# Kernel optimization log

Measured on AMD Instinct MI355X. Metric: run time of the kernel, lower is better.

Reference implementation:

```python
import jax, jax.numpy as jnp
import numpy as np

N = 50000      # nodes
E = 800000     # edges (self-loop-free; reference appends self loops like PyG GATv2Conv)
IN = 128; H = 4; C = 64; HC = H * C; HID = 64; OUT = 2


def _gat_conv(x, wl, bl, wr, br, att, bias, src, dst, n):
    # PyG GATv2Conv: e_ij = att . leaky_relu(W_l x_j + W_r x_i); segment softmax over dst;
    # out_i = sum_j alpha_ij * (W_l x_j), heads concatenated, plus bias.
    xl = (x @ wl + bl).reshape(n, H, C)
    xr = (x @ wr + br).reshape(n, H, C)
    e = jnp.sum(att * jax.nn.leaky_relu(xl[src] + xr[dst], 0.2), axis=-1)  # [E+n, H]
    m = jax.ops.segment_max(e, dst, num_segments=n)                         # [n, H]
    ex = jnp.exp(e - m[dst])
    s = jax.ops.segment_sum(ex, dst, num_segments=n)
    alpha = ex / (s[dst] + 1e-16)
    out = jax.ops.segment_sum(xl[src] * alpha[..., None], dst, num_segments=n)
    return out.reshape(n, HC) + bias


def _graph_norm(x, w, b, ms, eps=1e-5):
    # PyG GraphNorm, single graph: normalize over all nodes
    mean = jnp.mean(x, axis=0)
    xc = x - ms * mean
    var = jnp.mean(xc * xc, axis=0)
    return w * xc / jnp.sqrt(var + eps) + b


def setup_inputs() -> dict:
    key = jax.random.key(0)
    k = jax.random.split(key, 16)
    x = jax.random.normal(k[0], (N, IN), dtype=jnp.float32)
    src = jax.random.randint(k[1], (E,), 0, N, dtype=jnp.int32)
    dst = jax.random.randint(k[2], (E,), 0, N, dtype=jnp.int32)
    dst = jnp.where(dst == src, (dst + 1) % N, dst)  # no self loops in raw edges
    edge_index = jnp.stack([src, dst])

    def lin(kk, fi, fo):
        return (jax.random.normal(kk, (fi, fo), jnp.float32) / np.float32(np.sqrt(fi)))

    zeros = lambda d: jnp.zeros((d,), jnp.float32)
    ones = lambda d: jnp.ones((d,), jnp.float32)
    return dict(
        x=x, edge_index=edge_index,
        conv0_wl=lin(k[3], IN, HC), conv0_bl=zeros(HC),
        conv0_wr=lin(k[4], IN, HC), conv0_br=zeros(HC),
        conv0_att=jax.random.normal(k[5], (H, C), jnp.float32) / np.float32(np.sqrt(C)),
        conv0_bias=zeros(HC),
        conv1_wl=lin(k[6], HC, HC), conv1_bl=zeros(HC),
        conv1_wr=lin(k[7], HC, HC), conv1_br=zeros(HC),
        conv1_att=jax.random.normal(k[8], (H, C), jnp.float32) / np.float32(np.sqrt(C)),
        conv1_bias=zeros(HC),
        gn0_w=ones(HC), gn0_b=zeros(HC), gn0_ms=ones(HC),
        gn1_w=ones(HC), gn1_b=zeros(HC), gn1_ms=ones(HC),
        lin0_w=lin(k[9], HC, HID), lin0_b=zeros(HID),
        lin1_w=lin(k[10], HID, HID), lin1_b=zeros(HID),
        lin2_w=lin(k[11], HID, OUT), lin2_b=zeros(OUT),
    )


def reference(x, edge_index, conv0_wl, conv0_bl, conv0_wr, conv0_br, conv0_att, conv0_bias,
              conv1_wl, conv1_bl, conv1_wr, conv1_br, conv1_att, conv1_bias,
              gn0_w, gn0_b, gn0_ms, gn1_w, gn1_b, gn1_ms,
              lin0_w, lin0_b, lin1_w, lin1_b, lin2_w, lin2_b):
    n = x.shape[0]
    loop = jnp.arange(n, dtype=edge_index.dtype)
    src = jnp.concatenate([edge_index[0], loop])  # add self loops (PyG default)
    dst = jnp.concatenate([edge_index[1], loop])
    # NOTE: original forward zips convs (3) with norms (2) -> only 2 convs execute.
    h = _gat_conv(x, conv0_wl, conv0_bl, conv0_wr, conv0_br, conv0_att, conv0_bias, src, dst, n)
    h = jax.nn.relu(_graph_norm(h, gn0_w, gn0_b, gn0_ms))
    h = _gat_conv(h, conv1_wl, conv1_bl, conv1_wr, conv1_br, conv1_att, conv1_bias, src, dst, n)
    h = jax.nn.relu(_graph_norm(h, gn1_w, gn1_b, gn1_ms))
    h = jax.nn.relu(h @ lin0_w + lin0_b)  # dropout_rate=None -> no dropout
    h = jax.nn.relu(h @ lin1_w + lin1_b)
    return h @ lin2_w + lin2_b
```

## Files before the change

### kernel.cpp

```cpp
#include <hip/hip_runtime.h>
#include <hip/hip_bf16.h>


typedef __bf16 bf16x8 __attribute__((ext_vector_type(8)));
typedef float  f32x4  __attribute__((ext_vector_type(4)));

__device__ __forceinline__ unsigned short f2b(float f) {
    unsigned u = __float_as_uint(f);
    return (unsigned short)((u + 0x7fffu + ((u >> 16) & 1u)) >> 16);
}

__device__ __forceinline__ unsigned pk_norm(unsigned u, float a0, float a1,
                                            float c0, float c1) {
    float lo = __uint_as_float(u << 16);
    float hi = __uint_as_float(u & 0xffff0000u);
    lo = fmaxf(fmaf(a0, lo, c0), 0.f);
    hi = fmaxf(fmaf(a1, hi, c1), 0.f);
    unsigned r;
    asm volatile("v_cvt_pk_bf16_f32 %0, %1, %2" : "=v"(r) : "v"(lo), "v"(hi));
    return r;
}

__global__ __launch_bounds__(256) void prep_all(
    const float* __restrict__ x, unsigned short* __restrict__ xbf, int nx4,
    const float* __restrict__ w0l, const float* __restrict__ w0r, unsigned short* __restrict__ Wt0,
    const float* __restrict__ w1l, const float* __restrict__ w1r, unsigned short* __restrict__ Wt1,
    const float* __restrict__ l0, unsigned short* __restrict__ Lt0,
    const float* __restrict__ l1, unsigned short* __restrict__ Lt1,
    float* __restrict__ zf, int* __restrict__ hist, int nh)
{
    int t = blockIdx.x * 256 + threadIdx.x;
    if (t < 512) { zf[t] = 0.f; }
    int i = t - 512;
    if (i >= 0 && i < nh) hist[i] = 0;
    i -= nh;
    if (i >= 0 && i < nx4) {
        float4 v = ((const float4*)x)[i];
        ushort4 o = { f2b(v.x), f2b(v.y), f2b(v.z), f2b(v.w) };
        ((ushort4*)xbf)[i] = o;
    }
    i -= nx4;
    if (i >= 0 && i < 32768) { int nn = i >> 7, kk = i & 127; Wt0[i] = f2b(w0l[kk * 256 + nn]); }
    i -= 32768;
    if (i >= 0 && i < 32768) { int nn = i >> 7, kk = i & 127; Wt0[32768 + i] = f2b(w0r[kk * 256 + nn]); }
    i -= 32768;
    if (i >= 0 && i < 65536) { int nn = i >> 8, kk = i & 255; Wt1[i] = f2b(w1l[kk * 256 + nn]); }
    i -= 65536;
    if (i >= 0 && i < 65536) { int nn = i >> 8, kk = i & 255; Wt1[65536 + i] = f2b(w1r[kk * 256 + nn]); }
    i -= 65536;
    if (i >= 0 && i < 16384) { int nn = i >> 8, kk = i & 255; Lt0[i] = f2b(l0[kk * 64 + nn]); }
    i -= 16384;
    if (i >= 0 && i < 4096)  { int nn = i >> 6, kk = i & 63;  Lt1[i] = f2b(l1[kk * 64 + nn]); }
}

template<int K, bool RELU, bool NORM>
__global__ __launch_bounds__(256) void mfma_gemm(
    const unsigned short* __restrict__ A, const unsigned short* __restrict__ Bt,
    const float* __restrict__ bias0, const float* __restrict__ bias1, int split,
    const float* __restrict__ na, const float* __restrict__ nc,
    unsigned short* __restrict__ C, int M, int N, int nt)
{
    __shared__ unsigned short cs[256][72];

    const int nwg = gridDim.x;
    const int bid = blockIdx.x;
    const int q = nwg >> 3, r = nwg & 7;
    const int xcd = bid & 7, pos = bid >> 3;
    const int wgid = (xcd < r ? xcd * (q + 1) : r * (q + 1) + (xcd - r) * q) + pos;
    const int tm = wgid / nt;
    const int tn = wgid - tm * nt;

    const int lane = threadIdx.x & 63;
    const int w = threadIdx.x >> 6;
    const int bm = tm * 256 + w * 64;
    const int bn = tn * 64;
    const int lr = lane & 15;
    const int g  = lane >> 4;
    const int lk = g * 8;

    f32x4 acc[4][4] = {};
    const unsigned short* pa[4];
    #pragma unroll
    for (int mi = 0; mi < 4; ++mi) {
        int rr = bm + mi * 16 + lr;
        if (rr >= M) rr = M - 1;
        pa[mi] = A + (size_t)rr * K + lk;
    }
    const unsigned short* pb = Bt + (size_t)(bn + lr) * K + lk;

    #pragma unroll
    for (int k0 = 0; k0 < K; k0 += 32) {
        bf16x8 bfr[4], afr[4];
        #pragma unroll
        for (int ni = 0; ni < 4; ++ni)
            bfr[ni] = *(const bf16x8*)(pb + (size_t)ni * 16 * K + k0);
        if constexpr (NORM) {
            const float4 av0 = *(const float4*)(na + k0 + lk);
            const float4 av1 = *(const float4*)(na + k0 + lk + 4);
            const float4 cv0 = *(const float4*)(nc + k0 + lk);
            const float4 cv1 = *(const float4*)(nc + k0 + lk + 4);
            #pragma unroll
            for (int mi = 0; mi < 4; ++mi) {
                uint4 u = *(const uint4*)(pa[mi] + k0);
                uint4 rr;
                rr.x = pk_norm(u.x, av0.x, av0.y, cv0.x, cv0.y);
                rr.y = pk_norm(u.y, av0.z, av0.w, cv0.z, cv0.w);
                rr.z = pk_norm(u.z, av1.x, av1.y, cv1.x, cv1.y);
                rr.w = pk_norm(u.w, av1.z, av1.w, cv1.z, cv1.w);
                afr[mi] = __builtin_bit_cast(bf16x8, rr);
            }
        } else {
            #pragma unroll
            for (int mi = 0; mi < 4; ++mi)
                afr[mi] = *(const bf16x8*)(pa[mi] + k0);
        }
        #pragma unroll
        for (int mi = 0; mi < 4; ++mi)
            #pragma unroll
            for (int ni = 0; ni < 4; ++ni)
                acc[mi][ni] = __builtin_amdgcn_mfma_f32_16x16x32_bf16(
                    bfr[ni], afr[mi], acc[mi][ni], 0, 0, 0);
    }

    #pragma unroll
    for (int ni = 0; ni < 4; ++ni) {
        const int colbase = bn + ni * 16 + g * 4;
        const float4 bv = (colbase < split)
            ? *(const float4*)(bias0 + colbase)
            : *(const float4*)(bias1 + (colbase - split));
        #pragma unroll
        for (int mi = 0; mi < 4; ++mi) {
            float v0 = acc[mi][ni][0] + bv.x;
            float v1 = acc[mi][ni][1] + bv.y;
            float v2 = acc[mi][ni][2] + bv.z;
            float v3 = acc[mi][ni][3] + bv.w;
            if (RELU) {
                v0 = fmaxf(v0, 0.f); v1 = fmaxf(v1, 0.f);
                v2 = fmaxf(v2, 0.f); v3 = fmaxf(v3, 0.f);
            }
            ushort4 o = { f2b(v0), f2b(v1), f2b(v2), f2b(v3) };
            *(ushort4*)&cs[w * 64 + mi * 16 + lr][ni * 16 + g * 4] = o;
        }
    }
    __syncthreads();

    const int row32 = threadIdx.x >> 3;
    const int seg = threadIdx.x & 7;
    #pragma unroll
    for (int p = 0; p < 8; ++p) {
        const int lrow = p * 32 + row32;
        const int grow = tm * 256 + lrow;
        if (grow < M)
            *(uint4*)(C + (size_t)grow * N + bn + seg * 8) =
                *(const uint4*)&cs[lrow][seg * 8];
    }
}

__global__ void hist_kernel(const int* __restrict__ dst, int E, int* __restrict__ hist) {
    int e = blockIdx.x * 256 + threadIdx.x;
    if (e < E) atomicAdd(&hist[dst[e]], 1);
}

__global__ void blk_sum_kernel(const int* __restrict__ hist, int n, int* __restrict__ bsum) {
    __shared__ int lds[256];
    int t = threadIdx.x;
    int i = blockIdx.x * 256 + t;
    lds[t] = (i < n) ? hist[i] : 0;
    __syncthreads();
    for (int off = 128; off > 0; off >>= 1) {
        if (t < off) lds[t] += lds[t + off];
        __syncthreads();
    }
    if (t == 0) bsum[blockIdx.x] = lds[0];
}
__global__ void bsum_scan_kernel(int* __restrict__ bsum, int nblk,
                                 int* __restrict__ row_ptr, int n) {
    __shared__ int lds[256];
    int t = threadIdx.x;
    int v = (t < nblk) ? bsum[t] : 0;
    lds[t] = v;
    __syncthreads();
    for (int off = 1; off < 256; off <<= 1) {
        int u = (t >= off) ? lds[t - off] : 0;
        __syncthreads();
        lds[t] += u;
        __syncthreads();
    }
    if (t < nblk) bsum[t] = lds[t] - v;
    if (t == 255) row_ptr[n] = lds[255];
}
__global__ void final_scan_kernel(const int* __restrict__ hist, const int* __restrict__ bsum,
                                  int n, int* __restrict__ row_ptr, int* __restrict__ cursor) {
    __shared__ int lds[256];
    int t = threadIdx.x;
    int i = blockIdx.x * 256 + t;
    int v = (i < n) ? hist[i] : 0;
    lds[t] = v;
    __syncthreads();
    for (int off = 1; off < 256; off <<= 1) {
        int u = (t >= off) ? lds[t - off] : 0;
        __syncthreads();
        lds[t] += u;
        __syncthreads();
    }
    if (i < n) {
        int ex = bsum[blockIdx.x] + lds[t] - v;
        row_ptr[i] = ex;
        cursor[i] = ex;
    }
}

__global__ void scatter_kernel(const int* __restrict__ src, const int* __restrict__ dst,
                               int E, int* cursor, int* __restrict__ esrc)
{
    int e = blockIdx.x * 256 + threadIdx.x;
    if (e < E) {
        int pos = atomicAdd(&cursor[dst[e]], 1);
        esrc[pos] = src[e];
    }
}

template<int CTRL>
__device__ __forceinline__ float dppadd(float v) {
    return v + __int_as_float(__builtin_amdgcn_update_dpp(
        0, __float_as_int(v), CTRL, 0xf, 0xf, true));
}
__device__ __forceinline__ float red8(float v) {
    v = dppadd<0xB1>(v);
    v = dppadd<0x4E>(v);
    v = dppadd<0x141>(v);
    return v;
}
__device__ __forceinline__ f32x4 unpA(uint4 u) {
    f32x4 r;
    r.x = __uint_as_float(u.x << 16); r.y = __uint_as_float(u.y << 16);
    r.z = __uint_as_float(u.z << 16); r.w = __uint_as_float(u.w << 16);
    return r;
}
__device__ __forceinline__ f32x4 unpB(uint4 u) {
    f32x4 r;
    r.x = __uint_as_float(u.x & 0xffff0000u); r.y = __uint_as_float(u.y & 0xffff0000u);
    r.z = __uint_as_float(u.z & 0xffff0000u); r.w = __uint_as_float(u.w & 0xffff0000u);
    return r;
}

__global__ __launch_bounds__(256) void gat_aggregate(
    const unsigned short* __restrict__ xlr, const float* __restrict__ att,
    const int* __restrict__ row_ptr, const int* __restrict__ esrc,
    const float* __restrict__ bias, unsigned short* __restrict__ out, int n)
{
    const int lane = threadIdx.x & 63;
    const int node = __builtin_amdgcn_readfirstlane(blockIdx.x * 4 + (threadIdx.x >> 6));
    if (node >= n) return;
    const int sub = lane & 31;
    const int half = lane >> 5;
    const int c8 = sub * 8;

    const float LOG2E = 1.4426950408889634f;
    const float4 a0 = *(const float4*)(att + c8);
    const float4 a1 = *(const float4*)(att + c8 + 4);
    f32x4 attA = { a0.x, a0.z, a1.x, a1.z };
    f32x4 attB = { a0.y, a0.w, a1.y, a1.w };
    attA *= LOG2E; attB *= LOG2E;

    const uint4 xru = *(const uint4*)(xlr + (size_t)node * 512 + 256 + c8);
    const f32x4 xrA = unpA(xru), xrB = unpB(xru);

    float m = -1e30f, s = 0.f;
    f32x4 accA = {}, accB = {};

    const int start = row_ptr[node];
    const int cnt = row_ptr[node + 1] - start + 1;
    const int kmax = (cnt + 1) >> 1;

    int idx = half;
    int srcv = (idx == 0) ? node : ((idx < cnt) ? esrc[start + idx - 1] : node);
    uint4 nu = *(const uint4*)(xlr + (size_t)srcv * 512 + c8);

    for (int k = 0; k < kmax; ++k) {
        const f32x4 vA = unpA(nu), vB = unpB(nu);
        const float mask = (idx < cnt) ? 1.f : 0.f;
        const int idxn = idx + 2;
        const int srcn = (idxn < cnt) ? esrc[start + idxn - 1] : node;
        nu = *(const uint4*)(xlr + (size_t)srcn * 512 + c8);

        const f32x4 zA = vA + xrA, zB = vB + xrB;
        const f32x4 tA = __builtin_elementwise_max(zA, zA * 0.2f);
        const f32x4 tB = __builtin_elementwise_max(zB, zB * 0.2f);
        f32x4 p = attA * tA;
        p = __builtin_elementwise_fma(attB, tB, p);
        const float e = red8((p.x + p.z) + (p.y + p.w));

        const float d = e - m;
        if (__builtin_expect(__any(d > 8.f), 0)) {
            const float mn = fmaxf(m, e);
            const float cs = __builtin_amdgcn_exp2f(m - mn);
            const float w  = __builtin_amdgcn_exp2f(e - mn) * mask;
            s = fmaf(s, cs, w);
            const f32x4 w4 = { w, w, w, w }, cv = { cs, cs, cs, cs };
            accA = __builtin_elementwise_fma(accA, cv, w4 * vA);
            accB = __builtin_elementwise_fma(accB, cv, w4 * vB);
            m = mn;
        } else {
            const float w = __builtin_amdgcn_exp2f(d) * mask;
            s += w;
            const f32x4 w4 = { w, w, w, w };
            accA = __builtin_elementwise_fma(w4, vA, accA);
            accB = __builtin_elementwise_fma(w4, vB, accB);
        }
        idx = idxn;
    }

    const float m_o = __shfl_xor(m, 32);
    const float s_o = __shfl_xor(s, 32);
    f32x4 accAo, accBo;
    accAo.x = __shfl_xor(accA.x, 32); accAo.y = __shfl_xor(accA.y, 32);
    accAo.z = __shfl_xor(accA.z, 32); accAo.w = __shfl_xor(accA.w, 32);
    accBo.x = __shfl_xor(accB.x, 32); accBo.y = __shfl_xor(accB.y, 32);
    accBo.z = __shfl_xor(accB.z, 32); accBo.w = __shfl_xor(accB.w, 32);
    const float mn = fmaxf(m, m_o);
    const float c0 = __builtin_amdgcn_exp2f(m - mn);
    const float c1 = __builtin_amdgcn_exp2f(m_o - mn);
    const float st = s * c0 + s_o * c1;
    const float inv = 1.f / (st + 1e-16f);

    if (half == 0) {
        const f32x4 oA = (accA * c0 + accAo * c1) * inv;
        const f32x4 oB = (accB * c0 + accBo * c1) * inv;
        const float4 b0 = *(const float4*)(bias + c8);
        const float4 b1 = *(const float4*)(bias + c8 + 4);
        uint4 o;
        o.x = (unsigned)f2b(oA.x + b0.x) | ((unsigned)f2b(oB.x + b0.y) << 16);
        o.y = (unsigned)f2b(oA.y + b0.z) | ((unsigned)f2b(oB.y + b0.w) << 16);
        o.z = (unsigned)f2b(oA.z + b1.x) | ((unsigned)f2b(oB.z + b1.y) << 16);
        o.w = (unsigned)f2b(oA.w + b1.z) | ((unsigned)f2b(oB.w + b1.w) << 16);
        *(uint4*)(out + (size_t)node * 256 + c8) = o;
    }
}

__global__ __launch_bounds__(256) void colstats_bf16(
    const unsigned short* __restrict__ x, int n,
    float* __restrict__ sum, float* __restrict__ sumsq)
{
    const int c = threadIdx.x;
    float s = 0.f, q = 0.f;
    for (int r = blockIdx.x; r < n; r += gridDim.x) {
        float v = __uint_as_float(((unsigned)x[(size_t)r * 256 + c]) << 16);
        s += v;
        q = fmaf(v, v, q);
    }
    atomicAdd(&sum[c], s);
    atomicAdd(&sumsq[c], q);
}
__global__ void norm_finalize(float* __restrict__ sum, float* __restrict__ sumsq,
                              const float* __restrict__ w, const float* __restrict__ b,
                              const float* __restrict__ ms,
                              float* __restrict__ a, float* __restrict__ c2, float invn)
{
    int i = threadIdx.x;
    float mean = sum[i] * invn;
    float ex2 = sumsq[i] * invn;
    float m = ms[i];
    float var = ex2 - 2.f * m * mean * mean + m * m * mean * mean;
    float av = w[i] * rsqrtf(var + 1e-5f);
    a[i] = av;
    c2[i] = b[i] - av * m * mean;
    sum[i] = 0.f;
    sumsq[i] = 0.f;
}

__global__ void lin2_kernel(const unsigned short* __restrict__ h, const float* __restrict__ w,
                            const float* __restrict__ b, float* __restrict__ out, int n)
{
    int i = blockIdx.x * 256 + threadIdx.x;
    if (i >= n) return;
    float a0 = b[0], a1 = b[1];
    const unsigned short* hr = h + (size_t)i * 64;
    #pragma unroll
    for (int k = 0; k < 64; ++k) {
        float v = __uint_as_float(((unsigned)hr[k]) << 16);
        a0 = fmaf(v, w[k * 2 + 0], a0);
        a1 = fmaf(v, w[k * 2 + 1], a1);
    }
    out[i * 2 + 0] = a0;
    out[i * 2 + 1] = a1;
}

extern "C" void kernel_launch(void* const* d_in, const int* in_sizes, int n_in,
                              void* d_out, int out_size, void* d_ws, size_t ws_size,
                              hipStream_t stream)
{
    const float* x      = (const float*)d_in[0];
    const int*   eidx   = (const int*)d_in[1];
    const float* c0_wl  = (const float*)d_in[2];
    const float* c0_bl  = (const float*)d_in[3];
    const float* c0_wr  = (const float*)d_in[4];
    const float* c0_br  = (const float*)d_in[5];
    const float* c0_att = (const float*)d_in[6];
    const float* c0_bias= (const float*)d_in[7];
    const float* c1_wl  = (const float*)d_in[8];
    const float* c1_bl  = (const float*)d_in[9];
    const float* c1_wr  = (const float*)d_in[10];
    const float* c1_br  = (const float*)d_in[11];
    const float* c1_att = (const float*)d_in[12];
    const float* c1_bias= (const float*)d_in[13];
    const float* gn0_w  = (const float*)d_in[14];
    const float* gn0_b  = (const float*)d_in[15];
    const float* gn0_ms = (const float*)d_in[16];
    const float* gn1_w  = (const float*)d_in[17];
    const float* gn1_b  = (const float*)d_in[18];
    const float* gn1_ms = (const float*)d_in[19];
    const float* lin0_w = (const float*)d_in[20];
    const float* lin0_b = (const float*)d_in[21];
    const float* lin1_w = (const float*)d_in[22];
    const float* lin1_b = (const float*)d_in[23];
    const float* lin2_w = (const float*)d_in[24];
    const float* lin2_b = (const float*)d_in[25];

    const int n = in_sizes[0] / 128;
    const int E = in_sizes[1] / 2;
    const int* src = eidx;
    const int* dst = eidx + E;

    char* wsp = (char*)d_ws;
    size_t off = 0;
    auto alloc = [&](size_t bytes) -> void* {
        void* p = wsp + off;
        off = (off + bytes + 255) & ~(size_t)255;
        return p;
    };
    unsigned short* xbf  = (unsigned short*)alloc((size_t)n * 128 * 2);
    unsigned short* xlr  = (unsigned short*)alloc((size_t)n * 512 * 2);
    unsigned short* hbB  = (unsigned short*)alloc((size_t)n * 256 * 2);
    unsigned short* mbuf = (unsigned short*)alloc((size_t)n * 64 * 2);
    unsigned short* mbuf2= (unsigned short*)alloc((size_t)n * 64 * 2);
    unsigned short* Wt0  = (unsigned short*)alloc((size_t)512 * 128 * 2);
    unsigned short* Wt1  = (unsigned short*)alloc((size_t)512 * 256 * 2);
    unsigned short* Lt0  = (unsigned short*)alloc((size_t)64 * 256 * 2);
    unsigned short* Lt1  = (unsigned short*)alloc((size_t)64 * 64 * 2);
    int*   esrc    = (int*)alloc((size_t)E * 4);
    int*   row_ptr = (int*)alloc((size_t)(n + 1) * 4);
    int*   cursor  = (int*)alloc((size_t)n * 4);
    int*   hist    = (int*)alloc((size_t)n * 4);
    int*   bsum    = (int*)alloc((size_t)256 * 4);
    float* s_sum   = (float*)alloc(256 * 4);
    float* s_sq    = (float*)alloc(256 * 4);
    float* s_a     = (float*)alloc(256 * 4);
    float* s_c     = (float*)alloc(256 * 4);

    const int nx4 = n * 128 / 4;
    const int prep_total = 512 + n + nx4 + 32768 * 2 + 65536 * 2 + 16384 + 4096;
    prep_all<<<(prep_total + 255) / 256, 256, 0, stream>>>(
        x, xbf, nx4, c0_wl, c0_wr, Wt0, c1_wl, c1_wr, Wt1,
        lin0_w, Lt0, lin1_w, Lt1, s_sum, hist, n);

    const int nblk = (n + 255) / 256;
    hist_kernel<<<(E + 255) / 256, 256, 0, stream>>>(dst, E, hist);
    blk_sum_kernel<<<nblk, 256, 0, stream>>>(hist, n, bsum);
    bsum_scan_kernel<<<1, 256, 0, stream>>>(bsum, nblk, row_ptr, n);
    final_scan_kernel<<<nblk, 256, 0, stream>>>(hist, bsum, n, row_ptr, cursor);
    scatter_kernel<<<(E + 255) / 256, 256, 0, stream>>>(src, dst, E, cursor, esrc);

    const int mt = (n + 255) / 256;
    const int gagg = (n + 3) / 4;

    mfma_gemm<128, false, false><<<mt * 8, 256, 0, stream>>>(
        xbf, Wt0, c0_bl, c0_br, 256, nullptr, nullptr, xlr, n, 512, 8);
    gat_aggregate<<<gagg, 256, 0, stream>>>(xlr, c0_att, row_ptr, esrc, c0_bias, hbB, n);
    colstats_bf16<<<512, 256, 0, stream>>>(hbB, n, s_sum, s_sq);
    norm_finalize<<<1, 256, 0, stream>>>(s_sum, s_sq, gn0_w, gn0_b, gn0_ms, s_a, s_c, 1.f / n);

    mfma_gemm<256, false, true><<<mt * 8, 256, 0, stream>>>(
        hbB, Wt1, c1_bl, c1_br, 256, s_a, s_c, xlr, n, 512, 8);
    gat_aggregate<<<gagg, 256, 0, stream>>>(xlr, c1_att, row_ptr, esrc, c1_bias, hbB, n);
    colstats_bf16<<<512, 256, 0, stream>>>(hbB, n, s_sum, s_sq);
    norm_finalize<<<1, 256, 0, stream>>>(s_sum, s_sq, gn1_w, gn1_b, gn1_ms, s_a, s_c, 1.f / n);

    mfma_gemm<256, true, true><<<mt, 256, 0, stream>>>(
        hbB, Lt0, lin0_b, lin0_b, 64, s_a, s_c, mbuf, n, 64, 1);
    mfma_gemm<64, true, false><<<mt, 256, 0, stream>>>(
        mbuf, Lt1, lin1_b, lin1_b, 64, nullptr, nullptr, mbuf2, n, 64, 1);
    lin2_kernel<<<(n + 255) / 256, 256, 0, stream>>>(mbuf2, lin2_w, lin2_b, (float*)d_out, n);
}
```

Measured before the change: 439.6 us.

## Add 128x128-tile conv GEMM using direct global-to-LDS loads with swizzle

```diff
diff --git a/kernel.cpp b/kernel.cpp
--- a/kernel.cpp
+++ b/kernel.cpp
@@ -19,6 +19,12 @@
     unsigned r;
     asm volatile("v_cvt_pk_bf16_f32 %0, %1, %2" : "=v"(r) : "v"(lo), "v"(hi));
     return r;
+}
+
+__device__ __forceinline__ void gload_lds16(const unsigned short* g, unsigned short* l) {
+    __builtin_amdgcn_global_load_lds(
+        (const __attribute__((address_space(1))) unsigned int*)g,
+        (__attribute__((address_space(3))) unsigned int*)l, 16, 0, 0);
 }
 
 __global__ __launch_bounds__(256) void prep_all(
@@ -51,6 +57,115 @@
     if (i >= 0 && i < 16384) { int nn = i >> 8, kk = i & 255; Lt0[i] = f2b(l0[kk * 64 + nn]); }
     i -= 16384;
     if (i >= 0 && i < 4096)  { int nn = i >> 6, kk = i & 63;  Lt1[i] = f2b(l1[kk * 64 + nn]); }
+}
+
+template<int K, bool NORM>
+__global__ __launch_bounds__(256) void conv_gemm(
+    const unsigned short* __restrict__ A, const unsigned short* __restrict__ Bt,
+    const float* __restrict__ bias0, const float* __restrict__ bias1, int split,
+    const float* __restrict__ na, const float* __restrict__ nc,
+    unsigned short* __restrict__ C, int M, int N, int nt)
+{
+    __shared__ unsigned short smem[128 * 136];
+    unsigned short* sA = smem;
+    unsigned short* sB = smem + 4096;
+
+    const int nwg = gridDim.x;
+    const int bid = blockIdx.x;
+    const int q = nwg >> 3, r = nwg & 7;
+    const int xcd = bid & 7, pos = bid >> 3;
+    const int wgid = (xcd < r ? xcd * (q + 1) : r * (q + 1) + (xcd - r) * q) + pos;
+    const int tm = wgid / nt;
+    const int tn = wgid - tm * nt;
+
+    const int lane = threadIdx.x & 63;
+    const int w = threadIdx.x >> 6;
+    const int wm = w >> 1, wn = w & 1;
+    const int bm = tm * 128;
+    const int bn = tn * 128;
+    const int lr = lane & 15;
+    const int g  = lane >> 4;
+
+    const int srow = lane >> 2;
+    const int sk   = ((lane & 3) ^ (srow & 3)) << 3;
+    const int aslot = (g ^ (lr & 3)) << 3;
+
+    f32x4 acc[4][4] = {};
+
+    for (int k0 = 0; k0 < K; k0 += 32) {
+        #pragma unroll
+        for (int j = 0; j < 2; ++j) {
+            const int row = w * 32 + j * 16 + srow;
+            int ga = bm + row; if (ga >= M) ga = M - 1;
+            gload_lds16(A + (size_t)ga * K + k0 + sk, sA + (size_t)(w * 32 + j * 16) * 32);
+            gload_lds16(Bt + (size_t)(bn + row) * K + k0 + sk, sB + (size_t)(w * 32 + j * 16) * 32);
+        }
+        __syncthreads();
+
+        bf16x8 afr[4], bfr[4];
+        #pragma unroll
+        for (int mi = 0; mi < 4; ++mi) {
+            const int row = wm * 64 + mi * 16 + lr;
+            afr[mi] = *(const bf16x8*)(sA + row * 32 + aslot);
+        }
+        #pragma unroll
+        for (int ni = 0; ni < 4; ++ni) {
+            const int row = wn * 64 + ni * 16 + lr;
+            bfr[ni] = *(const bf16x8*)(sB + row * 32 + aslot);
+        }
+        if constexpr (NORM) {
+            const int lk = g * 8;
+            const float4 av0 = *(const float4*)(na + k0 + lk);
+            const float4 av1 = *(const float4*)(na + k0 + lk + 4);
+            const float4 cv0 = *(const float4*)(nc + k0 + lk);
+            const float4 cv1 = *(const float4*)(nc + k0 + lk + 4);
+            #pragma unroll
+            for (int mi = 0; mi < 4; ++mi) {
+                uint4 u = __builtin_bit_cast(uint4, afr[mi]);
+                uint4 rr;
+                rr.x = pk_norm(u.x, av0.x, av0.y, cv0.x, cv0.y);
+                rr.y = pk_norm(u.y, av0.z, av0.w, cv0.z, cv0.w);
+                rr.z = pk_norm(u.z, av1.x, av1.y, cv1.x, cv1.y);
+                rr.w = pk_norm(u.w, av1.z, av1.w, cv1.z, cv1.w);
+                afr[mi] = __builtin_bit_cast(bf16x8, rr);
+            }
+        }
+        #pragma unroll
+        for (int mi = 0; mi < 4; ++mi)
+            #pragma unroll
+            for (int ni = 0; ni < 4; ++ni)
+                acc[mi][ni] = __builtin_amdgcn_mfma_f32_16x16x32_bf16(
+                    bfr[ni], afr[mi], acc[mi][ni], 0, 0, 0);
+        __syncthreads();
+    }
+
+    unsigned short (*cs)[136] = (unsigned short(*)[136])smem;
+    #pragma unroll
+    for (int ni = 0; ni < 4; ++ni) {
+        const int lcol = wn * 64 + ni * 16 + g * 4;
+        const int col = bn + lcol;
+        const float4 bv = (col < split)
+            ? *(const float4*)(bias0 + col)
+            : *(const float4*)(bias1 + (col - split));
+        #pragma unroll
+        for (int mi = 0; mi < 4; ++mi) {
+            const int lrow = wm * 64 + mi * 16 + lr;
+            ushort4 o = { f2b(acc[mi][ni][0] + bv.x), f2b(acc[mi][ni][1] + bv.y),
+                          f2b(acc[mi][ni][2] + bv.z), f2b(acc[mi][ni][3] + bv.w) };
+            *(ushort4*)&cs[lrow][lcol] = o;
+        }
+    }
+    __syncthreads();
+    const int seg = threadIdx.x & 15;
+    const int rb  = threadIdx.x >> 4;
+    #pragma unroll
+    for (int p = 0; p < 8; ++p) {
+        const int lrow = p * 16 + rb;
+        const int grow = bm + lrow;
+        if (grow < M)
+            *(uint4*)(C + (size_t)grow * N + bn + seg * 8) =
+                *(const uint4*)&cs[lrow][seg * 8];
+    }
 }
 
 template<int K, bool RELU, bool NORM>
@@ -143,7 +258,6 @@
         }
     }
     __syncthreads();
-
     const int row32 = threadIdx.x >> 3;
     const int seg = threadIdx.x & 7;
     #pragma unroll
@@ -160,7 +274,6 @@
     int e = blockIdx.x * 256 + threadIdx.x;
     if (e < E) atomicAdd(&hist[dst[e]], 1);
 }
-
 __global__ void blk_sum_kernel(const int* __restrict__ hist, int n, int* __restrict__ bsum) {
     __shared__ int lds[256];
     int t = threadIdx.x;
@@ -209,7 +322,6 @@
         cursor[i] = ex;
     }
 }
-
 __global__ void scatter_kernel(const int* __restrict__ src, const int* __restrict__ dst,
                                int E, int* cursor, int* __restrict__ esrc)
 {
@@ -461,17 +573,18 @@
     final_scan_kernel<<<nblk, 256, 0, stream>>>(hist, bsum, n, row_ptr, cursor);
     scatter_kernel<<<(E + 255) / 256, 256, 0, stream>>>(src, dst, E, cursor, esrc);
 
-    const int mt = (n + 255) / 256;
+    const int mtc = (n + 127) / 128;
+    const int mt  = (n + 255) / 256;
     const int gagg = (n + 3) / 4;
 
-    mfma_gemm<128, false, false><<<mt * 8, 256, 0, stream>>>(
-        xbf, Wt0, c0_bl, c0_br, 256, nullptr, nullptr, xlr, n, 512, 8);
+    conv_gemm<128, false><<<mtc * 4, 256, 0, stream>>>(
+        xbf, Wt0, c0_bl, c0_br, 256, nullptr, nullptr, xlr, n, 512, 4);
     gat_aggregate<<<gagg, 256, 0, stream>>>(xlr, c0_att, row_ptr, esrc, c0_bias, hbB, n);
     colstats_bf16<<<512, 256, 0, stream>>>(hbB, n, s_sum, s_sq);
     norm_finalize<<<1, 256, 0, stream>>>(s_sum, s_sq, gn0_w, gn0_b, gn0_ms, s_a, s_c, 1.f / n);
 
-    mfma_gemm<256, false, true><<<mt * 8, 256, 0, stream>>>(
-        hbB, Wt1, c1_bl, c1_br, 256, s_a, s_c, xlr, n, 512, 8);
+    conv_gemm<256, true><<<mtc * 4, 256, 0, stream>>>(
+        hbB, Wt1, c1_bl, c1_br, 256, s_a, s_c, xlr, n, 512, 4);
     gat_aggregate<<<gagg, 256, 0, stream>>>(xlr, c1_att, row_ptr, esrc, c1_bias, hbB, n);
     colstats_bf16<<<512, 256, 0, stream>>>(hbB, n, s_sum, s_sq);
     norm_finalize<<<1, 256, 0, stream>>>(s_sum, s_sq, gn1_w, gn1_b, gn1_ms, s_a, s_c, 1.f / n);
```

After: 386.8 us. 12.0% less time.
